# Optimization experiments

Measured on AMD Instinct MI355X. Metric: run time of the kernel, lower is better.

## Reference

```python
import jax, jax.numpy as jnp
import numpy as np

B, NELEC, D, NION = 2048, 32, 128, 8
NSPIN = 2
NS = NELEC // NSPIN  # electrons (= orbitals) per spin


def setup_inputs() -> dict:
    key = jax.random.key(0)
    ks = jax.random.split(key, 6)
    eq_inputs = jax.random.normal(ks[0], (B, NELEC, D), dtype=jnp.float32)
    r_ei = jax.random.normal(ks[1], (B, NELEC, NION, 3), dtype=jnp.float32)
    W = jax.random.normal(ks[2], (NSPIN, D, NS), dtype=jnp.float32) / np.sqrt(D).astype(np.float32)
    b = jax.random.normal(ks[3], (NSPIN, NS), dtype=jnp.float32) * 0.1
    env_a = jax.random.normal(ks[4], (NSPIN, NION, NS), dtype=jnp.float32) * 0.5 + 1.0
    env_ion = jax.random.normal(ks[5], (NSPIN, NION, NS), dtype=jnp.float32) / np.sqrt(NION).astype(np.float32)
    return {"eq_inputs": eq_inputs, "r_ei": r_ei, "W": W, "b": b,
            "env_a": env_a, "env_ion": env_ion}


def _submatrix_row_indices(n):
    # idx[i, j] = row index kept at slot j after deleting row i
    j = np.arange(n - 1)
    idx = j[None, :] + (j[None, :] >= np.arange(n)[:, None])
    return jnp.asarray(idx)  # (n, n-1) int32


def reference(eq_inputs, r_ei, W, b, env_a, env_ion):
    # split into spins (equal split -> stack for vectorization)
    eq_s = jnp.stack(jnp.split(eq_inputs, NSPIN, axis=-2))   # (s,B,ns,d)
    rei_s = jnp.stack(jnp.split(r_ei, NSPIN, axis=-3))       # (s,B,ns,nion,3)

    # FermiNet orbital layer: linear part * isotropic exponential envelope
    linear = jnp.einsum("sbnd,sdo->sbno", eq_s, W) + b[:, None, None, :]
    dist = jnp.linalg.norm(rei_s, axis=-1)                   # (s,B,ns,nion)
    # exp(-||a (r - R)||) = exp(-|a| * ||r - R||) for isotropic scalar decay a
    exp_part = jnp.exp(-dist[..., None] * jnp.abs(env_a)[:, None, None, :, :])
    env = jnp.einsum("sbnio,sio->sbno", exp_part, env_ion)
    M = linear * env                                         # (s,B,ns,ns) square orbital matrices

    # slog cofactor antiequivariance along first column
    first = M[..., 0]                                        # (s,B,ns)
    osign = jnp.sign(first)
    olog = jnp.log(jnp.abs(first))
    y = M[..., 1:]                                           # delete column 0
    idx = _submatrix_row_indices(NS)
    sub = jnp.take(y, idx, axis=-2)                          # (s,B,ns,ns-1,ns-1): row i deleted
    csign, clog = jnp.linalg.slogdet(sub)                    # (s,B,ns)
    alt = jnp.asarray((-1.0) ** np.arange(NS), dtype=M.dtype)  # alternating signs (-1)^i
    a_sign = osign * csign * alt
    a_log = olog + clog

    # multiply equivariant inputs (slog form) by the per-particle antisymmetry
    out_sign = jnp.sign(eq_s) * a_sign[..., None]            # (s,B,ns,d)
    out_log = jnp.log(jnp.abs(eq_s)) + a_log[..., None]
    # stacked representation of the per-spin SLArrayList: (spin, {sign,log}, B, ns, d)
    return jnp.stack([out_sign, out_log], axis=1)
```

## Files before the change

### kernel.cpp

```cpp
#include <hip/hip_runtime.h>
#include <math.h>

#define NB 2048

typedef double dbl4 __attribute__((ext_vector_type(4)));

__device__ __forceinline__ float signf_(float x) {
    return (x > 0.0f) ? 1.0f : ((x < 0.0f) ? -1.0f : 0.0f);
}

__device__ __forceinline__ double fast_exp_neg(double y) {
    const double LOG2E  = 1.4426950408889634074;
    const double LN2_HI = 6.93147180369123816490e-01;
    const double LN2_LO = 1.90821492927058770002e-10;
    const double kd = __builtin_rint(y * LOG2E);
    double r = __builtin_fma(-kd, LN2_HI, y);
    r = __builtin_fma(-kd, LN2_LO, r);
    double p = 2.755731922398589e-7;
    p = __builtin_fma(p, r, 2.755731922398589e-6);
    p = __builtin_fma(p, r, 2.480158730158730e-5);
    p = __builtin_fma(p, r, 1.984126984126984e-4);
    p = __builtin_fma(p, r, 1.388888888888889e-3);
    p = __builtin_fma(p, r, 8.333333333333333e-3);
    p = __builtin_fma(p, r, 4.166666666666667e-2);
    p = __builtin_fma(p, r, 1.666666666666667e-1);
    p = __builtin_fma(p, r, 0.5);
    p = __builtin_fma(p, r, 1.0);
    p = __builtin_fma(p, r, 1.0);
    const long long ek = ((long long)(1023 + (int)kd)) << 52;
    return p * __longlong_as_double(ek);
}

__global__ __launch_bounds__(64, 4)
void slogcof_kernel(const float* __restrict__ eq,
                    const float* __restrict__ rei,
                    const float* __restrict__ Wm,
                    const float* __restrict__ bias,
                    const float* __restrict__ env_a,
                    const float* __restrict__ env_ion,
                    float* __restrict__ out)
{
    __shared__ double sM[16][18];
    __shared__ double sDist[16][8];
    __shared__ float  sA[2][16];

    const int l   = threadIdx.x;
    const int P   = blockIdx.x;
    const int s   = P >> 11;
    const int bb  = P & (NB - 1);

    const int o16 = l & 15;
    const int q4  = l >> 4;

    const float* eqp = eq + (size_t)bb * 4096 + s * 2048;

    #pragma unroll
    for (int rep = 0; rep < 2; ++rep) {
        const int n = (l >> 3) + rep * 8;
        const int i = l & 7;
        const float* rp = rei + (size_t)bb * 768 + s * 384 + n * 24 + i * 3;
        const double x = (double)rp[0], y = (double)rp[1], z = (double)rp[2];
        sDist[n][i] = sqrt(x * x + y * y + z * z);
    }

    double accv[4];
    {
        const float* Wp = Wm + s * 2048;
        dbl4 acc0 = {0.0, 0.0, 0.0, 0.0};
        dbl4 acc1 = {0.0, 0.0, 0.0, 0.0};
        #pragma unroll 8
        for (int i = 0; i < 32; i += 2) {
            const double a0 = (double)eqp[o16 * 128 + 4 * i + q4];
            const double b0 = (double)Wp[64 * i + l];
            acc0 = __builtin_amdgcn_mfma_f64_16x16x4f64(a0, b0, acc0, 0, 0, 0);
            const double a1 = (double)eqp[o16 * 128 + 4 * (i + 1) + q4];
            const double b1 = (double)Wp[64 * (i + 1) + l];
            acc1 = __builtin_amdgcn_mfma_f64_16x16x4f64(a1, b1, acc1, 0, 0, 0);
        }
        #pragma unroll
        for (int r = 0; r < 4; ++r) accv[r] = acc0[r] + acc1[r];
    }

    int rowi[4], coli[4];
    {
        dbl4 pr = {0.0, 0.0, 0.0, 0.0};
        dbl4 pc = {0.0, 0.0, 0.0, 0.0};
        pr = __builtin_amdgcn_mfma_f64_16x16x4f64((double)o16, 1.0, pr, 0, 0, 0);
        pc = __builtin_amdgcn_mfma_f64_16x16x4f64(1.0, (double)o16, pc, 0, 0, 0);
        #pragma unroll
        for (int r = 0; r < 4; ++r) {
            rowi[r] = ((int)pr[r]) >> 2;
            coli[r] = ((int)pc[r]) >> 2;
        }
    }

    __syncthreads();

    #pragma unroll
    for (int r = 0; r < 4; ++r) sM[rowi[r]][coli[r]] = accv[r];
    __syncthreads();

    {
        const double bd = (double)bias[s * 16 + o16];
        double lin[4], ev[4] = {0.0, 0.0, 0.0, 0.0};
        #pragma unroll
        for (int jj = 0; jj < 4; ++jj) lin[jj] = sM[4 * q4 + jj][o16];
        #pragma unroll
        for (int i = 0; i < 8; ++i) {
            const double ea = fabs((double)env_a[s * 128 + i * 16 + o16]);
            const double ei = (double)env_ion[s * 128 + i * 16 + o16];
            #pragma unroll
            for (int jj = 0; jj < 4; ++jj)
                ev[jj] += fast_exp_neg(-sDist[4 * q4 + jj][i] * ea) * ei;
        }
        #pragma unroll
        for (int jj = 0; jj < 4; ++jj)
            sM[4 * q4 + jj][o16] = (lin[jj] + bd) * ev[jj];
    }
    __syncthreads();

    {
        const int j = o16;
        double row[16];
        #pragma unroll
        for (int c = 0; c < 16; ++c) row[c] = sM[j][c];
        const double m0 = row[0];

        double logdet = 0.0;
        int dsign = 1;
        int used = 0;
        int mystep = -1;

        #pragma unroll
        for (int k = 0; k < 16; ++k) {
            unsigned key;
            {
                const float av = (float)fabs(row[k]);
                key = used ? (unsigned)j
                           : ((__float_as_uint(av) & 0xFFFFFFC0u) | 0x20u | (unsigned)j);
            }
            #pragma unroll
            for (int off = 8; off >= 1; off >>= 1) {
                const unsigned k2 = (unsigned)__shfl_xor((int)key, off, 16);
                if (k2 > key) key = k2;
            }
            const int p = (int)(key & 15u);
            const double pivv = __shfl(row[k], p, 16);
            logdet += (double)logf((float)fabs(pivv));
            if (pivv < 0.0) dsign = -dsign;
            else if (pivv == 0.0) dsign = 0;
            if (j == p) { used = 1; mystep = k; }
            const double minv = (pivv != 0.0) ? (1.0 / pivv) : 0.0;
            const double mul = row[k] * minv;
            const int upd = !used;
            #pragma unroll
            for (int c = k + 1; c < 16; ++c) {
                const double pv = __shfl(row[c], p, 16);
                if (upd) row[c] -= mul * pv;
            }
            if (upd) row[k] = mul;
        }

        int invc = 0;
        #pragma unroll
        for (int j2 = 0; j2 < 16; ++j2) {
            const int s2 = __shfl(mystep, j2, 16);
            if (j2 > j && mystep > s2) invc++;
        }
        #pragma unroll
        for (int off = 8; off >= 1; off >>= 1) invc += __shfl_xor(invc, off, 16);
        if (invc & 1) dsign = -dsign;

        double wv = 0.0;
        #pragma unroll
        for (int o = 0; o < 16; ++o) {
            double c0 = (mystep < o) ? (row[o] * wv) : 0.0;
            #pragma unroll
            for (int off = 8; off >= 1; off >>= 1) c0 += __shfl_xor(c0, off, 16);
            if (mystep == o) wv = (((o == 0) ? 1.0 : 0.0) - c0) / row[o];
        }
        double vv = 0.0;
        #pragma unroll
        for (int k = 15; k >= 0; --k) {
            double c0 = (mystep > k) ? (row[k] * vv) : 0.0;
            #pragma unroll
            for (int off = 8; off >= 1; off >>= 1) c0 += __shfl_xor(c0, off, 16);
            if (mystep == k) vv = wv - c0;
        }

        if (l < 16) {
            const double zj = vv;
            const float zs = (zj > 0.0) ? 1.0f : ((zj < 0.0) ? -1.0f : 0.0f);
            const float ms = (m0 > 0.0) ? 1.0f : ((m0 < 0.0) ? -1.0f : 0.0f);
            sA[0][j] = ms * (float)dsign * zs;
            sA[1][j] = logf((float)fabs(m0)) + (float)logdet + logf((float)fabs(zj));
        }
    }
    __syncthreads();

    float* op0 = out + (size_t)s * 8388608 + (size_t)bb * 2048;
    float* op1 = op0 + 4194304;
    #pragma unroll
    for (int it = 0; it < 8; ++it) {
        const int n  = it * 2 + (l >> 5);
        const int d0 = (l & 31) * 4;
        const float4 x = *reinterpret_cast<const float4*>(eqp + n * 128 + d0);
        const float a_s = sA[0][n];
        const float a_l = sA[1][n];
        float4 osg, olg;
        osg.x = signf_(x.x) * a_s;  olg.x = logf(fabsf(x.x)) + a_l;
        osg.y = signf_(x.y) * a_s;  olg.y = logf(fabsf(x.y)) + a_l;
        osg.z = signf_(x.z) * a_s;  olg.z = logf(fabsf(x.z)) + a_l;
        osg.w = signf_(x.w) * a_s;  olg.w = logf(fabsf(x.w)) + a_l;
        *reinterpret_cast<float4*>(op0 + n * 128 + d0) = osg;
        *reinterpret_cast<float4*>(op1 + n * 128 + d0) = olg;
    }
}

extern "C" void kernel_launch(void* const* d_in, const int* in_sizes, int n_in,
                              void* d_out, int out_size, void* d_ws, size_t ws_size,
                              hipStream_t stream) {
    (void)in_sizes; (void)n_in; (void)out_size; (void)d_ws; (void)ws_size;
    slogcof_kernel<<<dim3(4096), dim3(64), 0, stream>>>(
        (const float*)d_in[0],
        (const float*)d_in[1],
        (const float*)d_in[2],
        (const float*)d_in[3],
        (const float*)d_in[4],
        (const float*)d_in[5],
        (float*)d_out);
}
```

Measured before the change: 136.1 us.

## Fuse cofactor solve into Gauss-Jordan elimination on transposed matrix, use fast logs

The matrix is stored transposed, and the elimination becomes Gauss-Jordan: the pivot row is normalized and an augmented right-hand-side entry is carried along. This replaces the separate forward and backward triangular solves, each of which needed per-step shuffle reductions. The cofactor vector is then gathered through shared memory by pivot step. It also drops one barrier and switches logf to __logf, which trades some accuracy of the log for speed, including on the large output log.

```diff
diff --git a/kernel.cpp b/kernel.cpp
--- a/kernel.cpp
+++ b/kernel.cpp
@@ -40,8 +40,10 @@
                     const float* __restrict__ env_ion,
                     float* __restrict__ out)
 {
-    __shared__ double sM[16][18];
+    __shared__ double sLin[16][17];
+    __shared__ double sMT[16][17];
     __shared__ double sDist[16][8];
+    __shared__ double sZ[16];
     __shared__ float  sA[2][16];
 
     const int l   = threadIdx.x;
@@ -94,17 +96,15 @@
         }
     }
 
-    __syncthreads();
-
     #pragma unroll
-    for (int r = 0; r < 4; ++r) sM[rowi[r]][coli[r]] = accv[r];
+    for (int r = 0; r < 4; ++r) sLin[rowi[r]][coli[r]] = accv[r];
     __syncthreads();
 
     {
         const double bd = (double)bias[s * 16 + o16];
         double lin[4], ev[4] = {0.0, 0.0, 0.0, 0.0};
         #pragma unroll
-        for (int jj = 0; jj < 4; ++jj) lin[jj] = sM[4 * q4 + jj][o16];
+        for (int jj = 0; jj < 4; ++jj) lin[jj] = sLin[4 * q4 + jj][o16];
         #pragma unroll
         for (int i = 0; i < 8; ++i) {
             const double ea = fabs((double)env_a[s * 128 + i * 16 + o16]);
@@ -115,7 +115,7 @@
         }
         #pragma unroll
         for (int jj = 0; jj < 4; ++jj)
-            sM[4 * q4 + jj][o16] = (lin[jj] + bd) * ev[jj];
+            sMT[o16][4 * q4 + jj] = (lin[jj] + bd) * ev[jj];
     }
     __syncthreads();
 
@@ -123,13 +123,14 @@
         const int j = o16;
         double row[16];
         #pragma unroll
-        for (int c = 0; c < 16; ++c) row[c] = sM[j][c];
-        const double m0 = row[0];
+        for (int c = 0; c < 16; ++c) row[c] = sMT[j][c];
+        const double m0 = sMT[0][j];
+        double a = (j == 0) ? 1.0 : 0.0;
 
         double logdet = 0.0;
         int dsign = 1;
         int used = 0;
-        int mystep = -1;
+        int mystep = 0;
 
         #pragma unroll
         for (int k = 0; k < 16; ++k) {
@@ -146,19 +147,22 @@
             }
             const int p = (int)(key & 15u);
             const double pivv = __shfl(row[k], p, 16);
-            logdet += (double)logf((float)fabs(pivv));
+            logdet += (double)__logf((float)fabs(pivv));
             if (pivv < 0.0) dsign = -dsign;
             else if (pivv == 0.0) dsign = 0;
-            if (j == p) { used = 1; mystep = k; }
+            const int isp = (j == p);
+            if (isp) { used = 1; mystep = k; }
             const double minv = (pivv != 0.0) ? (1.0 / pivv) : 0.0;
-            const double mul = row[k] * minv;
-            const int upd = !used;
+            const double f = row[k];
             #pragma unroll
             for (int c = k + 1; c < 16; ++c) {
-                const double pv = __shfl(row[c], p, 16);
-                if (upd) row[c] -= mul * pv;
-            }
-            if (upd) row[k] = mul;
+                const double pr = __shfl(row[c], p, 16) * minv;
+                row[c] = isp ? pr : __builtin_fma(-f, pr, row[c]);
+            }
+            {
+                const double pa = __shfl(a, p, 16) * minv;
+                a = isp ? pa : __builtin_fma(-f, pa, a);
+            }
         }
 
         int invc = 0;
@@ -171,29 +175,15 @@
         for (int off = 8; off >= 1; off >>= 1) invc += __shfl_xor(invc, off, 16);
         if (invc & 1) dsign = -dsign;
 
-        double wv = 0.0;
-        #pragma unroll
-        for (int o = 0; o < 16; ++o) {
-            double c0 = (mystep < o) ? (row[o] * wv) : 0.0;
-            #pragma unroll
-            for (int off = 8; off >= 1; off >>= 1) c0 += __shfl_xor(c0, off, 16);
-            if (mystep == o) wv = (((o == 0) ? 1.0 : 0.0) - c0) / row[o];
-        }
-        double vv = 0.0;
-        #pragma unroll
-        for (int k = 15; k >= 0; --k) {
-            double c0 = (mystep > k) ? (row[k] * vv) : 0.0;
-            #pragma unroll
-            for (int off = 8; off >= 1; off >>= 1) c0 += __shfl_xor(c0, off, 16);
-            if (mystep == k) vv = wv - c0;
-        }
+        sZ[mystep] = a;
+        __syncthreads();
+        const double zj = sZ[j];
 
         if (l < 16) {
-            const double zj = vv;
             const float zs = (zj > 0.0) ? 1.0f : ((zj < 0.0) ? -1.0f : 0.0f);
             const float ms = (m0 > 0.0) ? 1.0f : ((m0 < 0.0) ? -1.0f : 0.0f);
             sA[0][j] = ms * (float)dsign * zs;
-            sA[1][j] = logf((float)fabs(m0)) + (float)logdet + logf((float)fabs(zj));
+            sA[1][j] = __logf((float)fabs(m0)) + (float)logdet + __logf((float)fabs(zj));
         }
     }
     __syncthreads();
@@ -208,10 +198,10 @@
         const float a_s = sA[0][n];
         const float a_l = sA[1][n];
         float4 osg, olg;
-        osg.x = signf_(x.x) * a_s;  olg.x = logf(fabsf(x.x)) + a_l;
-        osg.y = signf_(x.y) * a_s;  olg.y = logf(fabsf(x.y)) + a_l;
-        osg.z = signf_(x.z) * a_s;  olg.z = logf(fabsf(x.z)) + a_l;
-        osg.w = signf_(x.w) * a_s;  olg.w = logf(fabsf(x.w)) + a_l;
+        osg.x = signf_(x.x) * a_s;  olg.x = __logf(fabsf(x.x)) + a_l;
+        osg.y = signf_(x.y) * a_s;  olg.y = __logf(fabsf(x.y)) + a_l;
+        osg.z = signf_(x.z) * a_s;  olg.z = __logf(fabsf(x.z)) + a_l;
+        osg.w = signf_(x.w) * a_s;  olg.w = __logf(fabsf(x.w)) + a_l;
         *reinterpret_cast<float4*>(op0 + n * 128 + d0) = osg;
         *reinterpret_cast<float4*>(op1 + n * 128 + d0) = olg;
     }
```

Result: faster. 126.5 us (-7.1%).
